# Optimization experiments

Hardware: AMD Instinct MI355X
Metric: run time of the kernel (lower is better)

## Reference

```python
import jax, jax.numpy as jnp
import numpy as np

N_NODES, N_EDGES, B = 100000, 200000, 2048
ND, ED, HID, OUT, HEADS = 64, 16, 512, 512, 4

# dummy-graph topology: central node 0 -> features 1..6, plus self loops (GATv2 default)
D_SRC = jnp.array([0, 0, 0, 0, 0, 0, 0, 1, 2, 3, 4, 5, 6])
D_DST = jnp.array([1, 2, 3, 4, 5, 6, 0, 1, 2, 3, 4, 5, 6])


def setup_inputs() -> dict:
    key = jax.random.key(0)
    ks = jax.random.split(key, 40)
    p = lambda k, sh: (jax.random.normal(k, sh, dtype=jnp.float32) * 0.05)
    inp = {
        'x': jax.random.normal(ks[0], (N_NODES, ND), dtype=jnp.float32),
        'edge_index': jax.random.randint(ks[1], (2, N_EDGES), 0, N_NODES),
        'edge_attr': jax.random.normal(ks[2], (N_EDGES, ED), dtype=jnp.float32),
        'batch': jnp.sort(jax.random.randint(ks[3], (N_NODES,), 0, B)),
        'ecfp': jax.random.uniform(ks[4], (B, OUT), dtype=jnp.float32),
        'topo': jax.random.uniform(ks[5], (B, OUT), dtype=jnp.float32),
        'maccs': jax.random.uniform(ks[6], (B, OUT), dtype=jnp.float32),
        'estate': jax.random.uniform(ks[7], (B, OUT), dtype=jnp.float32),
        'rdkit2d': jax.random.normal(ks[8], (B, OUT), dtype=jnp.float32),
        'phar2d': jax.random.normal(ks[9], (B, OUT), dtype=jnp.float32),
        # GINEConv 1: nn = Linear(ND, HID); edge proj Linear(ED, ND)
        'g1_W': p(ks[10], (ND, HID)), 'g1_b': p(ks[11], (HID,)),
        'e1_W': p(ks[12], (ED, ND)), 'e1_b': p(ks[13], (ND,)),
        'bn1_g': jnp.ones((HID,), jnp.float32), 'bn1_b': jnp.zeros((HID,), jnp.float32),
        # GINEConv 2: nn = Linear(HID, OUT); edge proj Linear(ED, HID)
        'g2_W': p(ks[14], (HID, OUT)), 'g2_b': p(ks[15], (OUT,)),
        'e2_W': p(ks[16], (ED, HID)), 'e2_b': p(ks[17], (HID,)),
        'bn2_g': jnp.ones((OUT,), jnp.float32), 'bn2_b': jnp.zeros((OUT,), jnp.float32),
        # GATv2Conv 1: OUT -> HID, heads, concat=False
        'gat1_Wl': p(ks[18], (OUT, HEADS * HID)), 'gat1_bl': p(ks[19], (HEADS * HID,)),
        'gat1_Wr': p(ks[20], (OUT, HEADS * HID)), 'gat1_br': p(ks[21], (HEADS * HID,)),
        'gat1_att': p(ks[22], (HEADS, HID)), 'gat1_bias': p(ks[23], (HID,)),
        'bn3_g': jnp.ones((HID,), jnp.float32), 'bn3_b': jnp.zeros((HID,), jnp.float32),
        # GATv2Conv 2: HID -> HID
        'gat2_Wl': p(ks[24], (HID, HEADS * HID)), 'gat2_bl': p(ks[25], (HEADS * HID,)),
        'gat2_Wr': p(ks[26], (HID, HEADS * HID)), 'gat2_br': p(ks[27], (HEADS * HID,)),
        'gat2_att': p(ks[28], (HEADS, HID)), 'gat2_bias': p(ks[29], (HID,)),
        'bn4_g': jnp.ones((HID,), jnp.float32), 'bn4_b': jnp.zeros((HID,), jnp.float32),
        'fc_W': p(ks[30], (HID, 1)), 'fc_b': p(ks[31], (1,)),
    }
    return inp


def _bn_eval(h, g, b):
    # PyG BatchNorm in eval mode with fresh running stats (mean=0, var=1)
    return g * (h * (1.0 / np.sqrt(1.0 + 1e-5))) + b


def _gatv2(z, Wl, bl, Wr, br, att, bias):
    # z: [B, 7, Cin]; GATv2Conv with self-loops, concat=False (mean over heads)
    Bn, Nn, _ = z.shape
    Hh, Co = att.shape
    gl = (z @ Wl + bl).reshape(Bn, Nn, Hh, Co)  # source transform
    gr = (z @ Wr + br).reshape(Bn, Nn, Hh, Co)  # target transform
    e = jax.nn.leaky_relu(gl[:, D_SRC] + gr[:, D_DST], 0.2)  # [B, 13, H, Co]
    logits = jnp.einsum('behc,hc->beh', e, att)  # [B, 13, H]

    def seg_softmax(lg):
        m = jax.ops.segment_max(lg, D_DST, num_segments=7)
        ex = jnp.exp(lg - m[D_DST])
        s = jax.ops.segment_sum(ex, D_DST, num_segments=7)
        return ex / s[D_DST]

    alpha = jax.vmap(seg_softmax)(logits)  # [B, 13, H]
    msg = gl[:, D_SRC] * alpha[..., None]  # [B, 13, H, Co]
    out = jax.vmap(lambda mm: jax.ops.segment_sum(mm, D_DST, num_segments=7))(msg)
    return out.mean(axis=2) + bias  # [B, 7, Co]


def reference(x, edge_index, edge_attr, batch, ecfp, topo, maccs, estate, rdkit2d, phar2d,
              g1_W, g1_b, e1_W, e1_b, bn1_g, bn1_b,
              g2_W, g2_b, e2_W, e2_b, bn2_g, bn2_b,
              gat1_Wl, gat1_bl, gat1_Wr, gat1_br, gat1_att, gat1_bias, bn3_g, bn3_b,
              gat2_Wl, gat2_bl, gat2_Wr, gat2_br, gat2_att, gat2_bias, bn4_g, bn4_b,
              fc_W, fc_b):
    N = x.shape[0]
    Bg = ecfp.shape[0]
    src, dst = edge_index[0], edge_index[1]
    # GINEConv 1: msg = relu(x_j + W_e e), sum-aggr, out = Lin(x + aggr) (eps=0)
    m = jax.nn.relu(x[src] + (edge_attr @ e1_W + e1_b))
    h = (x + jax.ops.segment_sum(m, dst, num_segments=N)) @ g1_W + g1_b
    h = jax.nn.relu(_bn_eval(h, bn1_g, bn1_b))  # dropout = identity (eval)
    # GINEConv 2
    m2 = jax.nn.relu(h[src] + (edge_attr @ e2_W + e2_b))
    h2 = (h + jax.ops.segment_sum(m2, dst, num_segments=N)) @ g2_W + g2_b
    h2 = jax.nn.relu(_bn_eval(h2, bn2_g, bn2_b))
    # global mean pool
    sums = jax.ops.segment_sum(h2, batch, num_segments=Bg)
    cnts = jax.ops.segment_sum(jnp.ones((N,), h2.dtype), batch, num_segments=Bg)
    graph_out = sums / jnp.maximum(cnts, 1.0)[:, None]  # [B, OUT]
    # batched 7-node dummy graphs (node 0 = graph embedding, 1..6 = features)
    xn = jnp.stack([graph_out, ecfp, topo, maccs, estate, rdkit2d, phar2d], axis=1)
    z = _gatv2(xn, gat1_Wl, gat1_bl, gat1_Wr, gat1_br, gat1_att, gat1_bias)
    z = jax.nn.relu(_bn_eval(z, bn3_g, bn3_b))
    z = _gatv2(z, gat2_Wl, gat2_bl, gat2_Wr, gat2_br, gat2_att, gat2_bias)
    z = jax.nn.relu(_bn_eval(z, bn4_g, bn4_b))
    return z[:, 0, :] @ fc_W + fc_b  # [B, 1]
```

## Files before the change

### kernel.cpp

```cpp
#include <hip/hip_runtime.h>
#include <hip/hip_bf16.h>

#define N_NODESC 100000
#define N_EDGESC 200000
#define BG 2048
#define NDIM 64
#define EDIM 16

typedef __bf16 bf16x8 __attribute__((ext_vector_type(8)));
typedef float f32x4 __attribute__((ext_vector_type(4)));

static __device__ __forceinline__ float bn_inv() { return 0.9999950000374997f; }

static __device__ __forceinline__ float b2f(short s) {
    __hip_bfloat16 h = *(const __hip_bfloat16*)&s;
    return __bfloat162float(h);
}

__device__ __forceinline__ void gl2lds16(const void* g, void* l) {
    __builtin_amdgcn_global_load_lds(
        (const __attribute__((address_space(1))) unsigned int*)g,
        (__attribute__((address_space(3))) unsigned int*)l, 16, 0, 0);
}

__global__ void zero_f4(float4* __restrict__ p, int n4) {
    int i = blockIdx.x * 256 + threadIdx.x;
    if (i < n4) p[i] = make_float4(0.f, 0.f, 0.f, 0.f);
}
__global__ void zero_int(int* __restrict__ p, int n) {
    int i = blockIdx.x * 256 + threadIdx.x;
    if (i < n) p[i] = 0;
}
__global__ void zero_out(float* __restrict__ p, int n) {
    int i = blockIdx.x * 256 + threadIdx.x;
    if (i < n) p[i] = 0.f;
}

__global__ void hist_dst(const int* __restrict__ dst, int* __restrict__ deg) {
    int i = blockIdx.x * 256 + threadIdx.x;
    if (i < N_EDGESC) atomicAdd(&deg[dst[i]], 1);
}
__global__ void scan_bsums(const int* __restrict__ deg, int* __restrict__ bsum, int n) {
    __shared__ int ls[256];
    int b = blockIdx.x, t = threadIdx.x;
    int s = 0;
#pragma unroll
    for (int j = 0; j < 4; j++) {
        int i = b * 1024 + t * 4 + j;
        if (i < n) s += deg[i];
    }
    ls[t] = s;
    __syncthreads();
    for (int off = 128; off; off >>= 1) {
        if (t < off) ls[t] += ls[t + off];
        __syncthreads();
    }
    if (t == 0) bsum[b] = ls[0];
}
__global__ void scan_top(int* __restrict__ bsum, int nb, int* __restrict__ total) {
    if (threadIdx.x == 0) {
        int acc = 0;
        for (int i = 0; i < nb; i++) { int v = bsum[i]; bsum[i] = acc; acc += v; }
        *total = acc;
    }
}
__global__ void scan_final(const int* __restrict__ deg, const int* __restrict__ bsum,
                           int* __restrict__ rowptr, int* __restrict__ cursor, int n) {
    __shared__ int ls[256];
    int b = blockIdx.x, t = threadIdx.x;
    int v[4], s = 0;
#pragma unroll
    for (int j = 0; j < 4; j++) {
        int i = b * 1024 + t * 4 + j;
        v[j] = (i < n) ? deg[i] : 0;
        s += v[j];
    }
    ls[t] = s;
    __syncthreads();
    int run = s;
    for (int off = 1; off < 256; off <<= 1) {
        int add = (t >= off) ? ls[t - off] : 0;
        __syncthreads();
        ls[t] += add;
        __syncthreads();
    }
    int excl = ls[t] - run + bsum[b];
#pragma unroll
    for (int j = 0; j < 4; j++) {
        int i = b * 1024 + t * 4 + j;
        if (i < n) { rowptr[i] = excl; cursor[i] = excl; excl += v[j]; }
    }
}
__global__ void scatter_eid(const int* __restrict__ dst, int* __restrict__ cursor,
                            int* __restrict__ eid) {
    int e = blockIdx.x * 256 + threadIdx.x;
    if (e < N_EDGESC) {
        int p = atomicAdd(&cursor[dst[e]], 1);
        eid[p] = e;
    }
}

__global__ void transpose_w(const float* __restrict__ W, __hip_bfloat16* __restrict__ hi,
                            int K, int N) {
    __shared__ float t[64][65];
    int k0 = blockIdx.x * 64, n0 = blockIdx.y * 64;
    int tid = threadIdx.x, tx = tid & 63, ty = tid >> 6;
    for (int r = ty; r < 64; r += 4) t[r][tx] = W[(size_t)(k0 + r) * N + n0 + tx];
    __syncthreads();
    for (int r = ty; r < 64; r += 4)
        hi[(size_t)(n0 + r) * K + k0 + tx] = __float2bfloat16(t[tx][r]);
}

__global__ void concat_bias(const float* __restrict__ a, const float* __restrict__ b,
                            float* __restrict__ o) {
    int i = blockIdx.x * 256 + threadIdx.x;
    if (i < 2048) { o[i] = a[i]; o[2048 + i] = b[i]; }
}

#define G1_NPW 8
__global__ __launch_bounds__(256, 6) void gine1_gather(
    const float* __restrict__ x, const int* __restrict__ srcv, const float* __restrict__ ea,
    const float* __restrict__ e1W, const float* __restrict__ e1b,
    const int* __restrict__ rowptr, const int* __restrict__ eid,
    __hip_bfloat16* __restrict__ xin) {
    int tid = threadIdx.x;
    int wave = tid >> 6, lane = tid & 63;
    float wreg[16];
#pragma unroll
    for (int k = 0; k < 16; k++) wreg[k] = e1W[k * 64 + lane];
    float bb = e1b[lane];
    int nbase = (blockIdx.x * 4 + wave) * G1_NPW;
#pragma unroll 1
    for (int it = 0; it < G1_NPW; it++) {
        int n = nbase + it;
        if (n >= N_NODESC) return;
        float acc = x[(size_t)n * 64 + lane];
        int beg = rowptr[n], end = rowptr[n + 1];
        for (int idx = beg; idx < end; idx++) {
            int e = eid[idx], s = srcv[e];
            const float4* ef = (const float4*)(ea + (size_t)e * 16);
            float4 e0 = ef[0], e1 = ef[1], e2 = ef[2], e3 = ef[3];
            float p = bb;
            p = fmaf(e0.x, wreg[0], p);  p = fmaf(e0.y, wreg[1], p);
            p = fmaf(e0.z, wreg[2], p);  p = fmaf(e0.w, wreg[3], p);
            p = fmaf(e1.x, wreg[4], p);  p = fmaf(e1.y, wreg[5], p);
            p = fmaf(e1.z, wreg[6], p);  p = fmaf(e1.w, wreg[7], p);
            p = fmaf(e2.x, wreg[8], p);  p = fmaf(e2.y, wreg[9], p);
            p = fmaf(e2.z, wreg[10], p); p = fmaf(e2.w, wreg[11], p);
            p = fmaf(e3.x, wreg[12], p); p = fmaf(e3.y, wreg[13], p);
            p = fmaf(e3.z, wreg[14], p); p = fmaf(e3.w, wreg[15], p);
            acc += fmaxf(x[(size_t)s * 64 + lane] + p, 0.f);
        }
        xin[(size_t)n * 64 + lane] = __float2bfloat16(acc);
    }
}

#define G2_NPB 8
__global__ __launch_bounds__(256, 5) void gine2_gather(
    const __hip_bfloat16* __restrict__ h, const int* __restrict__ srcv,
    const float* __restrict__ ea, const float* __restrict__ e2W,
    const float* __restrict__ e2b, const int* __restrict__ rowptr,
    const int* __restrict__ eid, __hip_bfloat16* __restrict__ a2, int n0, int n1) {
    int tid = threadIdx.x;
    int c0 = tid * 2;
    float wreg[2][16], breg[2];
#pragma unroll
    for (int j = 0; j < 2; j++) {
        breg[j] = e2b[c0 + j];
#pragma unroll
        for (int k = 0; k < 16; k++) wreg[j][k] = e2W[k * 512 + c0 + j];
    }
    int nbase = n0 + blockIdx.x * G2_NPB;
#pragma unroll 1
    for (int it = 0; it < G2_NPB; it++) {
        int n = nbase + it;
        if (n >= n1) return;
        unsigned int hv = *(const unsigned int*)((const short*)(h + (size_t)n * 512) + c0);
        const __hip_bfloat16* hb = (const __hip_bfloat16*)&hv;
        float acc[2] = {__bfloat162float(hb[0]), __bfloat162float(hb[1])};
        int beg = rowptr[n], end = rowptr[n + 1];
        int idx = beg;
#pragma unroll 1
        for (; idx + 2 <= end; idx += 2) {
            int ei0 = eid[idx], ei1 = eid[idx + 1];
            int s0 = srcv[ei0], s1 = srcv[ei1];
            const float4* ef0 = (const float4*)(ea + (size_t)ei0 * 16);
            const float4* ef1 = (const float4*)(ea + (size_t)ei1 * 16);
            float4 a0 = ef0[0], a1 = ef0[1], a2v = ef0[2], a3 = ef0[3];
            float4 b0 = ef1[0], b1 = ef1[1], b2v = ef1[2], b3 = ef1[3];
            unsigned int sv0 = *(const unsigned int*)((const short*)(h + (size_t)s0 * 512) + c0);
            unsigned int sv1 = *(const unsigned int*)((const short*)(h + (size_t)s1 * 512) + c0);
            const __hip_bfloat16* sb0 = (const __hip_bfloat16*)&sv0;
            const __hip_bfloat16* sb1 = (const __hip_bfloat16*)&sv1;
#pragma unroll
            for (int j = 0; j < 2; j++) {
                float p = breg[j];
                p = fmaf(a0.x, wreg[j][0], p);  p = fmaf(a0.y, wreg[j][1], p);
                p = fmaf(a0.z, wreg[j][2], p);  p = fmaf(a0.w, wreg[j][3], p);
                p = fmaf(a1.x, wreg[j][4], p);  p = fmaf(a1.y, wreg[j][5], p);
                p = fmaf(a1.z, wreg[j][6], p);  p = fmaf(a1.w, wreg[j][7], p);
                p = fmaf(a2v.x, wreg[j][8], p); p = fmaf(a2v.y, wreg[j][9], p);
                p = fmaf(a2v.z, wreg[j][10], p);p = fmaf(a2v.w, wreg[j][11], p);
                p = fmaf(a3.x, wreg[j][12], p); p = fmaf(a3.y, wreg[j][13], p);
                p = fmaf(a3.z, wreg[j][14], p); p = fmaf(a3.w, wreg[j][15], p);
                acc[j] += fmaxf(__bfloat162float(sb0[j]) + p, 0.f);
                float q = breg[j];
                q = fmaf(b0.x, wreg[j][0], q);  q = fmaf(b0.y, wreg[j][1], q);
                q = fmaf(b0.z, wreg[j][2], q);  q = fmaf(b0.w, wreg[j][3], q);
                q = fmaf(b1.x, wreg[j][4], q);  q = fmaf(b1.y, wreg[j][5], q);
                q = fmaf(b1.z, wreg[j][6], q);  q = fmaf(b1.w, wreg[j][7], q);
                q = fmaf(b2v.x, wreg[j][8], q); q = fmaf(b2v.y, wreg[j][9], q);
                q = fmaf(b2v.z, wreg[j][10], q);q = fmaf(b2v.w, wreg[j][11], q);
                q = fmaf(b3.x, wreg[j][12], q); q = fmaf(b3.y, wreg[j][13], q);
                q = fmaf(b3.z, wreg[j][14], q); q = fmaf(b3.w, wreg[j][15], q);
                acc[j] += fmaxf(__bfloat162float(sb1[j]) + q, 0.f);
            }
        }
        if (idx < end) {
            int ei = eid[idx];
            int s = srcv[ei];
            const float4* ef = (const float4*)(ea + (size_t)ei * 16);
            float4 a0 = ef[0], a1 = ef[1], a2v = ef[2], a3 = ef[3];
            unsigned int sv = *(const unsigned int*)((const short*)(h + (size_t)s * 512) + c0);
            const __hip_bfloat16* sb = (const __hip_bfloat16*)&sv;
#pragma unroll
            for (int j = 0; j < 2; j++) {
                float p = breg[j];
                p = fmaf(a0.x, wreg[j][0], p);  p = fmaf(a0.y, wreg[j][1], p);
                p = fmaf(a0.z, wreg[j][2], p);  p = fmaf(a0.w, wreg[j][3], p);
                p = fmaf(a1.x, wreg[j][4], p);  p = fmaf(a1.y, wreg[j][5], p);
                p = fmaf(a1.z, wreg[j][6], p);  p = fmaf(a1.w, wreg[j][7], p);
                p = fmaf(a2v.x, wreg[j][8], p); p = fmaf(a2v.y, wreg[j][9], p);
                p = fmaf(a2v.z, wreg[j][10], p);p = fmaf(a2v.w, wreg[j][11], p);
                p = fmaf(a3.x, wreg[j][12], p); p = fmaf(a3.y, wreg[j][13], p);
                p = fmaf(a3.z, wreg[j][14], p); p = fmaf(a3.w, wreg[j][15], p);
                acc[j] += fmaxf(__bfloat162float(sb[j]) + p, 0.f);
            }
        }
        __hip_bfloat16 o[2];
        o[0] = __float2bfloat16(acc[0]);
        o[1] = __float2bfloat16(acc[1]);
        *(unsigned int*)((short*)(a2 + (size_t)(n - n0) * 512) + c0) = *(const unsigned int*)o;
    }
}

template <int MODE>
__global__ __launch_bounds__(256, 4) void mfma_gemm(
    const __hip_bfloat16* __restrict__ A, const __hip_bfloat16* __restrict__ Bhi,
    int M, int K, int N, const float* __restrict__ bias, const float* __restrict__ bng,
    const float* __restrict__ bnb, const int* __restrict__ batch,
    float* __restrict__ psum, __hip_bfloat16* __restrict__ Cout) {
    __shared__ __align__(16) short buf[16896];
    short* AsP = buf;
    short* BhP = buf + 8192;

    int nwg = gridDim.x * gridDim.y;
    int wg = blockIdx.x + gridDim.x * blockIdx.y;
    int q = nwg >> 3, r = nwg & 7;
    int xcd = wg & 7, idx = wg >> 3;
    int swz = (xcd < r) ? (xcd * (q + 1) + idx)
                        : (r * (q + 1) + (xcd - r) * q + idx);
    int bx = swz % gridDim.x, by = swz / gridDim.x;

    int r0 = by * 128;
    int n0 = bx * 128;
    int tid = threadIdx.x;
    int lane = tid & 63;
    int wv = tid >> 6;
    int wm = (wv >> 1) * 64, wn = (wv & 1) * 64;

    f32x4 acc[4][4];
#pragma unroll
    for (int i = 0; i < 4; i++)
#pragma unroll
        for (int j = 0; j < 4; j++) acc[i][j] = (f32x4){0.f, 0.f, 0.f, 0.f};

    int rowA0 = tid >> 2, cbA0 = tid & 3;
    int rowA1 = (tid + 256) >> 2;
    int gA0 = r0 + rowA0; if (gA0 >= M) gA0 = M - 1;
    int gA1 = r0 + rowA1; if (gA1 >= M) gA1 = M - 1;
    const __hip_bfloat16* pA0 = A + (size_t)gA0 * K + cbA0 * 8;
    const __hip_bfloat16* pA1 = A + (size_t)gA1 * K + cbA0 * 8;
    const __hip_bfloat16* pB0 = Bhi + (size_t)(n0 + rowA0) * K + cbA0 * 8;
    const __hip_bfloat16* pB1 = Bhi + (size_t)(n0 + rowA1) * K + cbA0 * 8;

    int fi = lane & 15, kb = (lane >> 4) * 8;
    for (int k0 = 0; k0 < K; k0 += 64) {
        __syncthreads();
#pragma unroll
        for (int hh = 0; hh < 2; hh++) {
            int kk = k0 + hh * 32;
            gl2lds16(pA0 + kk, AsP + hh * 4096 + wv * 512);
            gl2lds16(pA1 + kk, AsP + hh * 4096 + 2048 + wv * 512);
            gl2lds16(pB0 + kk, BhP + hh * 4096 + wv * 512);
            gl2lds16(pB1 + kk, BhP + hh * 4096 + 2048 + wv * 512);
        }
        __syncthreads();
#pragma unroll
        for (int ks = 0; ks < 2; ks++) {
            bf16x8 af[4], bhf[4];
#pragma unroll
            for (int mi = 0; mi < 4; mi++)
                af[mi] = *(const bf16x8*)(AsP + ks * 4096 + (wm + mi * 16 + fi) * 32 + kb);
#pragma unroll
            for (int ni = 0; ni < 4; ni++)
                bhf[ni] = *(const bf16x8*)(BhP + ks * 4096 + (wn + ni * 16 + fi) * 32 + kb);
#pragma unroll
            for (int mi = 0; mi < 4; mi++)
#pragma unroll
                for (int ni = 0; ni < 4; ni++)
                    acc[mi][ni] = __builtin_amdgcn_mfma_f32_16x16x32_bf16(
                        af[mi], bhf[ni], acc[mi][ni], 0, 0, 0);
        }
    }
    int col_l = lane & 15, quad = lane >> 4;
    if (MODE == 0 || MODE == 1) {
        __syncthreads();
#pragma unroll
        for (int mi = 0; mi < 4; mi++) {
            int rloc = wm + mi * 16 + quad * 4;
#pragma unroll
            for (int ni = 0; ni < 4; ni++) {
                int cloc = wn + ni * 16 + col_l;
                float b0 = bias[n0 + cloc];
                float g0 = 0.f, bb0 = 0.f;
                if (MODE == 1) { g0 = bng[n0 + cloc]; bb0 = bnb[n0 + cloc]; }
#pragma unroll
                for (int reg = 0; reg < 4; reg++) {
                    float v = acc[mi][ni][reg] + b0;
                    if (MODE == 1) v = fmaxf(fmaf(v * bn_inv(), g0, bb0), 0.f);
                    __hip_bfloat16 hv = __float2bfloat16(v);
                    buf[(rloc + reg) * 132 + cloc] = *(const short*)&hv;
                }
            }
        }
        __syncthreads();
#pragma unroll
        for (int p = 0; p < 16; p++) {
            int row = p * 8 + (tid >> 5);
            int grow = r0 + row;
            if (grow < M) {
                int c4 = (tid & 31) * 4;
                unsigned long long v = *(const unsigned long long*)(buf + row * 132 + c4);
                unsigned long long* dst =
                    (unsigned long long*)(Cout + (size_t)grow * N + n0 + c4);
                if (MODE == 0) __builtin_nontemporal_store(v, dst);
                else *dst = v;
            }
        }
    } else {
#pragma unroll
        for (int mi = 0; mi < 4; mi++) {
            int rbase = r0 + wm + mi * 16 + quad * 4;
#pragma unroll
            for (int ni = 0; ni < 4; ni++) {
                int gcol = n0 + wn + ni * 16 + col_l;
                float b0 = bias[gcol], g0 = bng[gcol], bb0 = bnb[gcol];
                float vv[4];
#pragma unroll
                for (int reg = 0; reg < 4; reg++)
                    vv[reg] = fmaxf(fmaf((acc[mi][ni][reg] + b0) * bn_inv(), g0, bb0), 0.f);
                int rtop = r0 + wm + mi * 16;
                bool uni16 = (rtop + 15 < M) && (batch[rtop] == batch[rtop + 15]);
                float vs = (vv[0] + vv[1]) + (vv[2] + vv[3]);
                if (uni16) {
                    vs += __shfl_xor(vs, 16);
                    vs += __shfl_xor(vs, 32);
                    if (quad == 0)
                        atomicAdd(&psum[(size_t)batch[rtop] * 512 + gcol], vs);
                } else if (rbase + 3 < M && batch[rbase] == batch[rbase + 3]) {
                    atomicAdd(&psum[(size_t)batch[rbase] * 512 + gcol], vs);
                } else {
#pragma unroll
                    for (int reg = 0; reg < 4; reg++) {
                        int grow = rbase + reg;
                        if (grow < M)
                            atomicAdd(&psum[(size_t)batch[grow] * 512 + gcol], vv[reg]);
                    }
                }
            }
        }
    }
}

__global__ void count_nodes(const int* __restrict__ batch, float* __restrict__ cnt) {
    int i = blockIdx.x * 256 + threadIdx.x;
    if (i < N_NODESC) atomicAdd(&cnt[batch[i]], 1.0f);
}

__global__ void build_xn(const float* __restrict__ psum, const float* __restrict__ cnt,
                         const float* __restrict__ ecfp, const float* __restrict__ topo,
                         const float* __restrict__ maccs, const float* __restrict__ estate,
                         const float* __restrict__ rdkit2d, const float* __restrict__ phar2d,
                         __hip_bfloat16* __restrict__ xn) {
    int i = blockIdx.x * 256 + threadIdx.x;
    if (i >= BG * 512) return;
    int bidx = i >> 9, c = i & 511;
    float cv = fmaxf(cnt[bidx], 1.0f);
    __hip_bfloat16* o = xn + (size_t)bidx * 7 * 512;
    o[c] = __float2bfloat16(psum[i] / cv);
    o[512 + c] = __float2bfloat16(ecfp[i]);
    o[2 * 512 + c] = __float2bfloat16(topo[i]);
    o[3 * 512 + c] = __float2bfloat16(maccs[i]);
    o[4 * 512 + c] = __float2bfloat16(estate[i]);
    o[5 * 512 + c] = __float2bfloat16(rdkit2d[i]);
    o[6 * 512 + c] = __float2bfloat16(phar2d[i]);
}

__global__ void gat_attn(const __hip_bfloat16* __restrict__ cg,
                         const float* __restrict__ att, const float* __restrict__ bias,
                         const float* __restrict__ bng, const float* __restrict__ bnb,
                         __hip_bfloat16* __restrict__ zout) {
    int b = blockIdx.x;
    int tid = threadIdx.x;
    int wave = tid >> 6, lane = tid & 63;
    __shared__ float logits[13][4];
    __shared__ float alpha[13][4];
    const size_t base = (size_t)b * 7 * 4096;
    for (int p = wave; p < 52; p += 4) {
        int e = p >> 2, hh = p & 3;
        int se = (e < 7) ? 0 : (e - 6);
        int de = (e < 6) ? (e + 1) : ((e == 6) ? 0 : (e - 6));
        const short* glp = (const short*)(cg + base + (size_t)se * 4096 + hh * 512) + lane * 8;
        const short* grp = (const short*)(cg + base + (size_t)de * 4096 + 2048 + hh * 512) + lane * 8;
        short4 gl0 = ((const short4*)glp)[0], gl1 = ((const short4*)glp)[1];
        short4 gr0 = ((const short4*)grp)[0], gr1 = ((const short4*)grp)[1];
        const float4* ap = (const float4*)(att + hh * 512 + lane * 8);
        float4 a0 = ap[0], a1 = ap[1];
        float s = 0.f, v;
        v = b2f(gl0.x) + b2f(gr0.x); v = (v >= 0.f) ? v : 0.2f * v; s = fmaf(v, a0.x, s);
        v = b2f(gl0.y) + b2f(gr0.y); v = (v >= 0.f) ? v : 0.2f * v; s = fmaf(v, a0.y, s);
        v = b2f(gl0.z) + b2f(gr0.z); v = (v >= 0.f) ? v : 0.2f * v; s = fmaf(v, a0.z, s);
        v = b2f(gl0.w) + b2f(gr0.w); v = (v >= 0.f) ? v : 0.2f * v; s = fmaf(v, a0.w, s);
        v = b2f(gl1.x) + b2f(gr1.x); v = (v >= 0.f) ? v : 0.2f * v; s = fmaf(v, a1.x, s);
        v = b2f(gl1.y) + b2f(gr1.y); v = (v >= 0.f) ? v : 0.2f * v; s = fmaf(v, a1.y, s);
        v = b2f(gl1.z) + b2f(gr1.z); v = (v >= 0.f) ? v : 0.2f * v; s = fmaf(v, a1.z, s);
        v = b2f(gl1.w) + b2f(gr1.w); v = (v >= 0.f) ? v : 0.2f * v; s = fmaf(v, a1.w, s);
#pragma unroll
        for (int off = 32; off; off >>= 1) s += __shfl_down(s, off);
        if (lane == 0) logits[e][hh] = s;
    }
    __syncthreads();
    if (tid < 24) {
        int n = 1 + (tid >> 2), hh = tid & 3;
        float la = logits[n - 1][hh], lb = logits[6 + n][hh];
        float m = fmaxf(la, lb);
        float ea = __expf(la - m), eb = __expf(lb - m);
        float inv = 1.f / (ea + eb);
        alpha[n - 1][hh] = ea * inv;
        alpha[6 + n][hh] = eb * inv;
    } else if (tid < 28) {
        alpha[6][tid & 3] = 1.f;
    }
    __syncthreads();
    for (int u = tid; u < 7 * 128; u += 256) {
        int n = u >> 7, c4 = (u & 127) * 4;
        float v0 = 0.f, v1 = 0.f, v2 = 0.f, v3 = 0.f;
        const short* g0 = (const short*)(cg + base) + c4;
        if (n == 0) {
#pragma unroll
            for (int hh = 0; hh < 4; hh++) {
                short4 t = *(const short4*)(g0 + hh * 512);
                float a = alpha[6][hh];
                v0 = fmaf(a, b2f(t.x), v0); v1 = fmaf(a, b2f(t.y), v1);
                v2 = fmaf(a, b2f(t.z), v2); v3 = fmaf(a, b2f(t.w), v3);
            }
        } else {
            const short* gn = (const short*)(cg + base + (size_t)n * 4096) + c4;
#pragma unroll
            for (int hh = 0; hh < 4; hh++) {
                short4 t = *(const short4*)(g0 + hh * 512);
                float a = alpha[n - 1][hh];
                v0 = fmaf(a, b2f(t.x), v0); v1 = fmaf(a, b2f(t.y), v1);
                v2 = fmaf(a, b2f(t.z), v2); v3 = fmaf(a, b2f(t.w), v3);
                short4 t2 = *(const short4*)(gn + hh * 512);
                float a2 = alpha[6 + n][hh];
                v0 = fmaf(a2, b2f(t2.x), v0); v1 = fmaf(a2, b2f(t2.y), v1);
                v2 = fmaf(a2, b2f(t2.z), v2); v3 = fmaf(a2, b2f(t2.w), v3);
            }
        }
        float4 bi = *(const float4*)(bias + c4);
        float4 gg = *(const float4*)(bng + c4);
        float4 bb = *(const float4*)(bnb + c4);
        v0 = fmaxf(fmaf(fmaf(v0, 0.25f, bi.x) * bn_inv(), gg.x, bb.x), 0.f);
        v1 = fmaxf(fmaf(fmaf(v1, 0.25f, bi.y) * bn_inv(), gg.y, bb.y), 0.f);
        v2 = fmaxf(fmaf(fmaf(v2, 0.25f, bi.z) * bn_inv(), gg.z, bb.z), 0.f);
        v3 = fmaxf(fmaf(fmaf(v3, 0.25f, bi.w) * bn_inv(), gg.w, bb.w), 0.f);
        __hip_bfloat16 o[4];
        o[0] = __float2bfloat16(v0); o[1] = __float2bfloat16(v1);
        o[2] = __float2bfloat16(v2); o[3] = __float2bfloat16(v3);
        *(short4*)((short*)(zout + (size_t)b * 7 * 512) + n * 512 + c4) = *(const short4*)o;
    }
}

__global__ void final_fc(const __hip_bfloat16* __restrict__ z, const float* __restrict__ fcW,
                         const float* __restrict__ fcb, float* __restrict__ out) {
    int b = blockIdx.x * 4 + (threadIdx.x >> 6);
    int lane = threadIdx.x & 63;
    if (b >= BG) return;
    const __hip_bfloat16* row = z + (size_t)b * 7 * 512;
    float s = 0.f;
#pragma unroll
    for (int j = 0; j < 8; j++)
        s = fmaf(__bfloat162float(row[lane + j * 64]), fcW[lane + j * 64], s);
#pragma unroll
    for (int off = 32; off; off >>= 1) s += __shfl_down(s, off);
    if (lane == 0) out[b] = s + fcb[0];
}

extern "C" void kernel_launch(void* const* d_in, const int* in_sizes, int n_in,
                              void* d_out, int out_size, void* d_ws, size_t ws_size,
                              hipStream_t stream) {
    const float* x = (const float*)d_in[0];
    const int* eidx = (const int*)d_in[1];
    const float* eattr = (const float*)d_in[2];
    const int* batch = (const int*)d_in[3];
    const float* ecfp = (const float*)d_in[4];
    const float* topo = (const float*)d_in[5];
    const float* maccs = (const float*)d_in[6];
    const float* estate = (const float*)d_in[7];
    const float* rdkit2d = (const float*)d_in[8];
    const float* phar2d = (const float*)d_in[9];
    const float* g1_W = (const float*)d_in[10];
    const float* g1_b = (const float*)d_in[11];
    const float* e1_W = (const float*)d_in[12];
    const float* e1_b = (const float*)d_in[13];
    const float* bn1_g = (const float*)d_in[14];
    const float* bn1_b = (const float*)d_in[15];
    const float* g2_W = (const float*)d_in[16];
    const float* g2_b = (const float*)d_in[17];
    const float* e2_W = (const float*)d_in[18];
    const float* e2_b = (const float*)d_in[19];
    const float* bn2_g = (const float*)d_in[20];
    const float* bn2_b = (const float*)d_in[21];
    const float* gat1_Wl = (const float*)d_in[22];
    const float* gat1_bl = (const float*)d_in[23];
    const float* gat1_Wr = (const float*)d_in[24];
    const float* gat1_br = (const float*)d_in[25];
    const float* gat1_att = (const float*)d_in[26];
    const float* gat1_bias = (const float*)d_in[27];
    const float* bn3_g = (const float*)d_in[28];
    const float* bn3_b = (const float*)d_in[29];
    const float* gat2_Wl = (const float*)d_in[30];
    const float* gat2_bl = (const float*)d_in[31];
    const float* gat2_Wr = (const float*)d_in[32];
    const float* gat2_br = (const float*)d_in[33];
    const float* gat2_att = (const float*)d_in[34];
    const float* gat2_bias = (const float*)d_in[35];
    const float* bn4_g = (const float*)d_in[36];
    const float* bn4_b = (const float*)d_in[37];
    const float* fc_W = (const float*)d_in[38];
    const float* fc_b = (const float*)d_in[39];
    float* out = (float*)d_out;

    const size_t NEEDED = 194682880ull;
    if (ws_size < NEEDED) {
        zero_out<<<(BG + 255) / 256, 256, 0, stream>>>(out, BG);
        return;
    }
    char* w = (char*)d_ws;
    __hip_bfloat16* H = (__hip_bfloat16*)w;
    __hip_bfloat16* CG = (__hip_bfloat16*)w;
    __hip_bfloat16* A2 = (__hip_bfloat16*)(w + 102400000);
    __hip_bfloat16* GW12 = (__hip_bfloat16*)(w + 117440512);
    __hip_bfloat16* GW34 = (__hip_bfloat16*)(w + 121634816);
    __hip_bfloat16* Z1B = (__hip_bfloat16*)(w + 125829120);
    float* B12 = (float*)(w + 140509184);
    float* B34 = (float*)(w + 140525568);

    char* C = w + 161120256;
    __hip_bfloat16* XIN = (__hip_bfloat16*)C;
    __hip_bfloat16* XNB = (__hip_bfloat16*)C;
    __hip_bfloat16* Z2B = (__hip_bfloat16*)(C + 14680064);
    int* ROWPTR = (int*)(C + 14680064);
    int* CURSOR = (int*)(C + 15080192);
    int* EID = (int*)(C + 15480320);
    int* DEG = (int*)(C + 16280320);
    __hip_bfloat16* G1W = (__hip_bfloat16*)(C + 16680320);
    __hip_bfloat16* G2W = (__hip_bfloat16*)(C + 16745856);
    int* BSUM = (int*)(C + 17270144);

    float* PS = (float*)(w + 190480384);
    float* PC = (float*)(w + 194674688);

    const int* src = eidx;
    const int* dst = eidx + N_EDGESC;

    zero_int<<<(N_NODESC + 255) / 256, 256, 0, stream>>>(DEG, N_NODESC);
    zero_f4<<<(BG * 512 / 4 + 255) / 256, 256, 0, stream>>>((float4*)PS, BG * 512 / 4);
    zero_f4<<<(BG / 4 + 255) / 256, 256, 0, stream>>>((float4*)PC, BG / 4);
    hist_dst<<<(N_EDGESC + 255) / 256, 256, 0, stream>>>(dst, DEG);
    const int NB = (N_NODESC + 1023) / 1024;
    scan_bsums<<<NB, 256, 0, stream>>>(DEG, BSUM, N_NODESC);
    scan_top<<<1, 64, 0, stream>>>(BSUM, NB, ROWPTR + N_NODESC);
    scan_final<<<NB, 256, 0, stream>>>(DEG, BSUM, ROWPTR, CURSOR, N_NODESC);
    scatter_eid<<<(N_EDGESC + 255) / 256, 256, 0, stream>>>(dst, CURSOR, EID);

    transpose_w<<<dim3(1, 8), 256, 0, stream>>>(g1_W, G1W, 64, 512);
    transpose_w<<<dim3(8, 8), 256, 0, stream>>>(g2_W, G2W, 512, 512);

    gine1_gather<<<(N_NODESC + 4 * G1_NPW - 1) / (4 * G1_NPW), 256, 0, stream>>>(
        x, src, eattr, e1_W, e1_b, ROWPTR, EID, XIN);
    mfma_gemm<1><<<dim3(4, (N_NODESC + 127) / 128), 256, 0, stream>>>(
        XIN, G1W, N_NODESC, 64, 512, g1_b, bn1_g, bn1_b, nullptr, nullptr, H);
    count_nodes<<<(N_NODESC + 255) / 256, 256, 0, stream>>>(batch, PC);

    for (int c0n = 0; c0n < N_NODESC; c0n += 50000) {
        int c1n = c0n + 50000;
        int rows = 50000;
        gine2_gather<<<(rows + G2_NPB - 1) / G2_NPB, 256, 0, stream>>>(
            H, src, eattr, e2_W, e2_b, ROWPTR, EID, A2, c0n, c1n);
        mfma_gemm<2><<<dim3(4, (rows + 127) / 128), 256, 0, stream>>>(
            A2, G2W, rows, 512, 512, g2_b, bn2_g, bn2_b, batch + c0n, PS, nullptr);
    }

    transpose_w<<<dim3(8, 32), 256, 0, stream>>>(gat1_Wl, GW12, 512, 2048);
    transpose_w<<<dim3(8, 32), 256, 0, stream>>>(gat1_Wr, GW12 + (size_t)2048 * 512, 512, 2048);
    transpose_w<<<dim3(8, 32), 256, 0, stream>>>(gat2_Wl, GW34, 512, 2048);
    transpose_w<<<dim3(8, 32), 256, 0, stream>>>(gat2_Wr, GW34 + (size_t)2048 * 512, 512, 2048);
    concat_bias<<<8, 256, 0, stream>>>(gat1_bl, gat1_br, B12);
    concat_bias<<<8, 256, 0, stream>>>(gat2_bl, gat2_br, B34);

    build_xn<<<(BG * 512) / 256, 256, 0, stream>>>(PS, PC, ecfp, topo, maccs, estate,
                                                   rdkit2d, phar2d, XNB);
    const int MGAT = BG * 7;
    dim3 ggrid(4096 / 128, MGAT / 128);
    mfma_gemm<0><<<ggrid, 256, 0, stream>>>(XNB, GW12, MGAT, 512, 4096, B12,
                                            nullptr, nullptr, nullptr, nullptr, CG);
    gat_attn<<<BG, 256, 0, stream>>>(CG, gat1_att, gat1_bias, bn3_g, bn3_b, Z1B);
    mfma_gemm<0><<<ggrid, 256, 0, stream>>>(Z1B, GW34, MGAT, 512, 4096, B34,
                                            nullptr, nullptr, nullptr, nullptr, CG);
    gat_attn<<<BG, 256, 0, stream>>>(CG, gat2_att, gat2_bias, bn4_g, bn4_b, Z2B);
    final_fc<<<BG / 4, 256, 0, stream>>>(Z2B, fc_W, fc_b, out);
}
```

Measured before the change: 848.5 us.

## Double-buffer LDS tiles in MFMA GEMM to overlap loads with compute

The GEMM K loop is restructured from a load-sync-compute pattern over 64-wide K chunks into a double-buffered pipeline over 32-wide K tiles. The first tile is prefetched before the loop, and each iteration issues the async global-to-LDS loads for the next tile before running the MFMAs on the current one. This is meant to hide global-load latency behind matrix math. In exchange, each tile is smaller and there is still one barrier per 32-wide K step, so the number of barriers is unchanged. Correctness relies on the barrier also waiting for the outstanding async LDS loads.

```diff
diff --git a/kernel.cpp b/kernel.cpp
--- a/kernel.cpp
+++ b/kernel.cpp
@@ -251,8 +251,6 @@
     const float* __restrict__ bnb, const int* __restrict__ batch,
     float* __restrict__ psum, __hip_bfloat16* __restrict__ Cout) {
     __shared__ __align__(16) short buf[16896];
-    short* AsP = buf;
-    short* BhP = buf + 8192;
 
     int nwg = gridDim.x * gridDim.y;
     int wg = blockIdx.x + gridDim.x * blockIdx.y;
@@ -285,33 +283,38 @@
     const __hip_bfloat16* pB1 = Bhi + (size_t)(n0 + rowA1) * K + cbA0 * 8;
 
     int fi = lane & 15, kb = (lane >> 4) * 8;
-    for (int k0 = 0; k0 < K; k0 += 64) {
+    const int NT = K >> 5;
+    {
+        gl2lds16(pA0, buf + wv * 512);
+        gl2lds16(pA1, buf + 2048 + wv * 512);
+        gl2lds16(pB0, buf + 8192 + wv * 512);
+        gl2lds16(pB1, buf + 8192 + 2048 + wv * 512);
+    }
+#pragma unroll 1
+    for (int t = 0; t < NT; t++) {
         __syncthreads();
-#pragma unroll
-        for (int hh = 0; hh < 2; hh++) {
-            int kk = k0 + hh * 32;
-            gl2lds16(pA0 + kk, AsP + hh * 4096 + wv * 512);
-            gl2lds16(pA1 + kk, AsP + hh * 4096 + 2048 + wv * 512);
-            gl2lds16(pB0 + kk, BhP + hh * 4096 + wv * 512);
-            gl2lds16(pB1 + kk, BhP + hh * 4096 + 2048 + wv * 512);
-        }
-        __syncthreads();
-#pragma unroll
-        for (int ks = 0; ks < 2; ks++) {
-            bf16x8 af[4], bhf[4];
-#pragma unroll
-            for (int mi = 0; mi < 4; mi++)
-                af[mi] = *(const bf16x8*)(AsP + ks * 4096 + (wm + mi * 16 + fi) * 32 + kb);
+        int cur = (t & 1) * 4096;
+        if (t + 1 < NT) {
+            int nxt = ((t + 1) & 1) * 4096;
+            int kk = (t + 1) << 5;
+            gl2lds16(pA0 + kk, buf + nxt + wv * 512);
+            gl2lds16(pA1 + kk, buf + nxt + 2048 + wv * 512);
+            gl2lds16(pB0 + kk, buf + 8192 + nxt + wv * 512);
+            gl2lds16(pB1 + kk, buf + 8192 + nxt + 2048 + wv * 512);
+        }
+        bf16x8 af[4], bhf[4];
+#pragma unroll
+        for (int mi = 0; mi < 4; mi++)
+            af[mi] = *(const bf16x8*)(buf + cur + (wm + mi * 16 + fi) * 32 + kb);
+#pragma unroll
+        for (int ni = 0; ni < 4; ni++)
+            bhf[ni] = *(const bf16x8*)(buf + 8192 + cur + (wn + ni * 16 + fi) * 32 + kb);
+#pragma unroll
+        for (int mi = 0; mi < 4; mi++)
 #pragma unroll
             for (int ni = 0; ni < 4; ni++)
-                bhf[ni] = *(const bf16x8*)(BhP + ks * 4096 + (wn + ni * 16 + fi) * 32 + kb);
-#pragma unroll
-            for (int mi = 0; mi < 4; mi++)
-#pragma unroll
-                for (int ni = 0; ni < 4; ni++)
-                    acc[mi][ni] = __builtin_amdgcn_mfma_f32_16x16x32_bf16(
-                        af[mi], bhf[ni], acc[mi][ni], 0, 0, 0);
-        }
+                acc[mi][ni] = __builtin_amdgcn_mfma_f32_16x16x32_bf16(
+                    af[mi], bhf[ni], acc[mi][ni], 0, 0, 0);
     }
     int col_l = lane & 15, quad = lane >> 4;
     if (MODE == 0 || MODE == 1) {
```

New measurement: 843.3 us. Within noise of the previous version (-0.6%).
